# Kernel optimization log

Measured on AMD Instinct MI355X. Metric: run time of the kernel, lower is better.

## Reference

```python
import jax, jax.numpy as jnp
import numpy as np

N, F_IN, HID, HEADS, E, NG = 50000, 128, 64, 4, 800000, 64
NEG_SLOPE = 0.2


def gat_conv(x, src, dst, W, a_src, a_dst, bias, heads, out_ch, concat):
    n = x.shape[0]
    h = (x @ W).reshape(n, heads, out_ch)                     # [N,H,C]
    # per-node attention logits
    al_src = jnp.sum(h * a_src, axis=-1)                      # [N,H]
    al_dst = jnp.sum(h * a_dst, axis=-1)                      # [N,H]
    e = jax.nn.leaky_relu(al_src[src] + al_dst[dst], NEG_SLOPE)  # [E,H]
    # segment softmax over incoming edges of each destination node
    m = jax.ops.segment_max(e, dst, num_segments=n)           # [N,H]
    m = jnp.where(jnp.isfinite(m), m, 0.0)
    ex = jnp.exp(e - m[dst])
    denom = jax.ops.segment_sum(ex, dst, num_segments=n)      # [N,H]
    alpha = ex / (denom[dst] + 1e-16)                         # [E,H]
    # weighted scatter-sum of gathered source features
    out = jax.ops.segment_sum(h[src] * alpha[:, :, None], dst, num_segments=n)  # [N,H,C]
    if concat:
        out = out.reshape(n, heads * out_ch)
    else:
        out = out.mean(axis=1)
    return out + bias


def setup_inputs() -> dict:
    key = jax.random.key(0)
    ks = jax.random.split(key, 16)
    x = jax.random.normal(ks[0], (N, F_IN), dtype=jnp.float32)
    edge_index = jax.random.randint(ks[1], (2, E), 0, N, dtype=jnp.int32)
    batch = jnp.sort(jax.random.randint(ks[2], (N,), 0, NG, dtype=jnp.int32))
    s1 = 1.0 / np.sqrt(F_IN)
    s2 = 1.0 / np.sqrt(HID * HEADS)
    W1 = jax.random.uniform(ks[3], (F_IN, HEADS * HID), jnp.float32, -s1, s1)
    a_src1 = jax.random.uniform(ks[4], (HEADS, HID), jnp.float32, -s1, s1)
    a_dst1 = jax.random.uniform(ks[5], (HEADS, HID), jnp.float32, -s1, s1)
    b1 = jnp.zeros((HEADS * HID,), jnp.float32)
    W2 = jax.random.uniform(ks[6], (HEADS * HID, HID), jnp.float32, -s2, s2)
    a_src2 = jax.random.uniform(ks[7], (1, HID), jnp.float32, -s2, s2)
    a_dst2 = jax.random.uniform(ks[8], (1, HID), jnp.float32, -s2, s2)
    b2 = jnp.zeros((HID,), jnp.float32)
    s3 = 1.0 / np.sqrt(HID)
    fcW = jax.random.uniform(ks[9], (HID, 1), jnp.float32, -s3, s3)
    fcb = jax.random.uniform(ks[10], (1,), jnp.float32, -s3, s3)
    return {"x": x, "edge_index": edge_index, "batch": batch,
            "W1": W1, "a_src1": a_src1, "a_dst1": a_dst1, "b1": b1,
            "W2": W2, "a_src2": a_src2, "a_dst2": a_dst2, "b2": b2,
            "fcW": fcW, "fcb": fcb}


def reference(x, edge_index, batch, W1, a_src1, a_dst1, b1, W2, a_src2, a_dst2, b2, fcW, fcb):
    n = x.shape[0]
    # PyG GATConv default: add self-loops
    loop = jnp.arange(n, dtype=edge_index.dtype)
    src = jnp.concatenate([edge_index[0], loop])
    dst = jnp.concatenate([edge_index[1], loop])
    # dropout layers are identity at inference
    h = gat_conv(x, src, dst, W1, a_src1, a_dst1, b1, HEADS, HID, True)
    h = jax.nn.elu(h)
    h = gat_conv(h, src, dst, W2, a_src2, a_dst2, b2, 1, HID, False)
    h = jax.nn.elu(h)
    # global mean pool over graphs
    sums = jax.ops.segment_sum(h, batch, num_segments=NG)      # [NG,HID]
    cnts = jax.ops.segment_sum(jnp.ones((n,), h.dtype), batch, num_segments=NG)
    pooled = sums / jnp.maximum(cnts, 1.0)[:, None]
    out = pooled @ fcW + fcb                                    # [NG,1]
    return out.squeeze(-1)
```

## Files before the change

kernel.cpp:

```cpp
#include <hip/hip_runtime.h>
#include <hip/hip_fp16.h>
#include <cstddef>
#include <cstdint>


#define LOG2E 1.4426950408889634f
__device__ __forceinline__ float lrelu02(float x) { return x >= 0.f ? x : 0.2f * x; }
__device__ __forceinline__ float elu1(float x)    { return x > 0.f ? x : expm1f(x); }
__device__ __forceinline__ float fexp(float x)    { return exp2f(x * LOG2E); }

typedef _Float16 f16x8 __attribute__((ext_vector_type(8)));
typedef float    f32x4 __attribute__((ext_vector_type(4)));

__global__ void k_hist(const int* __restrict__ dst, int* __restrict__ cnt,
                       int* __restrict__ rank, int e) {
    int i = blockIdx.x * 256 + threadIdx.x;
    if (i < e) rank[i] = atomicAdd(&cnt[dst[i]], 1);
}

__global__ __launch_bounds__(1024) void k_scan1(const int* __restrict__ cnt,
                                                int* __restrict__ cscan,
                                                int* __restrict__ bsum, int n) {
    __shared__ int ws[16];
    const int t = threadIdx.x, lane = t & 63, wv = t >> 6;
    const int i = blockIdx.x * 1024 + t;
    int v = (i < n) ? cnt[i] : 0;
    int s = v;
#pragma unroll
    for (int d = 1; d < 64; d <<= 1) { int o = __shfl_up(s, d); if (lane >= d) s += o; }
    if (lane == 63) ws[wv] = s;
    __syncthreads();
    if (t < 16) {
        int xx = ws[t];
#pragma unroll
        for (int d = 1; d < 16; d <<= 1) { int o = __shfl_up(xx, d); if (t >= d) xx += o; }
        ws[t] = xx;
        if (t == 15) bsum[blockIdx.x] = xx;
    }
    __syncthreads();
    int incl = s + (wv > 0 ? ws[wv - 1] : 0);
    if (i < n) cscan[i] = incl;
}

__global__ __launch_bounds__(1024) void k_scan2(int* __restrict__ bsum, int nb) {
    __shared__ int ws[16];
    const int t = threadIdx.x, lane = t & 63, wv = t >> 6;
    int v = (t < nb) ? bsum[t] : 0;
    int s = v;
#pragma unroll
    for (int d = 1; d < 64; d <<= 1) { int o = __shfl_up(s, d); if (lane >= d) s += o; }
    if (lane == 63) ws[wv] = s;
    __syncthreads();
    if (t < 16) {
        int xx = ws[t];
#pragma unroll
        for (int d = 1; d < 16; d <<= 1) { int o = __shfl_up(xx, d); if (t >= d) xx += o; }
        ws[t] = xx;
    }
    __syncthreads();
    int incl = s + (wv > 0 ? ws[wv - 1] : 0);
    if (t < nb) bsum[t] = incl - v;
}

__global__ __launch_bounds__(1024) void k_scan3(const int* __restrict__ cscan,
                                                const int* __restrict__ bsum,
                                                int* __restrict__ rowptr, int n) {
    const int i = blockIdx.x * 1024 + threadIdx.x;
    if (i < n) rowptr[i + 1] = cscan[i] + bsum[blockIdx.x];
    if (i == 0) rowptr[0] = 0;
}

__global__ void k_scatter(const int* __restrict__ src, const int* __restrict__ dstArr,
                          const int* __restrict__ rank, const int* __restrict__ rowptr,
                          int* __restrict__ csr, int e) {
    int i = blockIdx.x * 256 + threadIdx.x;
    if (i < e) csr[rowptr[dstArr[i]] + rank[i]] = src[i];
}

__device__ __forceinline__ void packOne(const float* __restrict__ W, __half* __restrict__ Bp,
                                        int K, int N, int i) {
    int c = i & 15, q = (i >> 4) & 3, tnt = i >> 6;
    int nt = tnt % (N / 16), t = tnt / (N / 16);
    int k0 = t * 32 + q * 8, col = nt * 16 + c;
    __half tmp[8];
#pragma unroll
    for (int j = 0; j < 8; ++j) tmp[j] = __float2half(W[(size_t)(k0 + j) * N + col]);
    *reinterpret_cast<int4*>(Bp + (size_t)i * 8) = *reinterpret_cast<int4*>(tmp);
}

__global__ void k_packW(const float* __restrict__ W1, __half* __restrict__ B1,
                        const float* __restrict__ W2, __half* __restrict__ B2) {
    int i = blockIdx.x * 256 + threadIdx.x;
    if (i < 4096) packOne(W1, B1, 128, 256, i);
    else if (i < 4096 + 2048) packOne(W2, B2, 256, 64, i - 4096);
}

template <int K, int N, bool AF32, int HEADS_>
__global__ __launch_bounds__(256) void k_gemm_mfma(const void* __restrict__ Av,
                                                   const __half* __restrict__ Bp,
                                                   __half* __restrict__ C,
                                                   const float* __restrict__ a_src,
                                                   const float* __restrict__ a_dst,
                                                   float* __restrict__ als,
                                                   float* __restrict__ ald, int M) {
    constexpr int NT = N / 16, KT = K / 32;
    const int lane = threadIdx.x & 63;
    const int wv = threadIdx.x >> 6;
    const int row0 = (blockIdx.x * 4 + wv) * 16;
    if (row0 >= M) return;

    f32x4 acc[NT];
#pragma unroll
    for (int nt = 0; nt < NT; ++nt) acc[nt] = (f32x4){0.f, 0.f, 0.f, 0.f};

    const __half* Ah = (const __half*)Av;
    const float*  Af = (const float*)Av;
    const size_t arow = (size_t)(row0 + (lane & 15)) * K + (lane >> 4) * 8;
    const __half* Bb = Bp + (size_t)lane * 8;
#pragma unroll
    for (int t = 0; t < KT; ++t) {
        f16x8 a;
        if constexpr (AF32) {
            float4 u0 = *reinterpret_cast<const float4*>(Af + arow + t * 32);
            float4 u1 = *reinterpret_cast<const float4*>(Af + arow + t * 32 + 4);
            a[0] = (_Float16)u0.x; a[1] = (_Float16)u0.y;
            a[2] = (_Float16)u0.z; a[3] = (_Float16)u0.w;
            a[4] = (_Float16)u1.x; a[5] = (_Float16)u1.y;
            a[6] = (_Float16)u1.z; a[7] = (_Float16)u1.w;
        } else {
            a = *reinterpret_cast<const f16x8*>(Ah + arow + t * 32);
        }
#pragma unroll
        for (int nt = 0; nt < NT; ++nt) {
            f16x8 b = *reinterpret_cast<const f16x8*>(Bb + (size_t)(t * NT + nt) * 512);
            acc[nt] = __builtin_amdgcn_mfma_f32_16x16x32_f16(a, b, acc[nt], 0, 0, 0);
        }
    }
    const int r0 = row0 + (lane >> 4) * 4;
    const int cl = lane & 15;
#pragma unroll
    for (int nt = 0; nt < NT; ++nt) {
        int col = nt * 16 + cl;
#pragma unroll
        for (int j = 0; j < 4; ++j)
            C[(size_t)(r0 + j) * N + col] = __float2half(acc[nt][j]);
    }
    float av[NT], dv[NT];
#pragma unroll
    for (int nt = 0; nt < NT; ++nt) {
        av[nt] = a_src[nt * 16 + cl];
        dv[nt] = a_dst[nt * 16 + cl];
    }
    constexpr int NTH = NT / HEADS_;
#pragma unroll
    for (int j = 0; j < 4; ++j) {
#pragma unroll
        for (int h = 0; h < HEADS_; ++h) {
            float ps = 0.f, pd = 0.f;
#pragma unroll
            for (int t = 0; t < NTH; ++t) {
                ps = fmaf(acc[h * NTH + t][j], av[h * NTH + t], ps);
                pd = fmaf(acc[h * NTH + t][j], dv[h * NTH + t], pd);
            }
#pragma unroll
            for (int d = 1; d < 16; d <<= 1) { ps += __shfl_xor(ps, d); pd += __shfl_xor(pd, d); }
            if (cl == 0) {
                int r = r0 + j;
                als[(size_t)r * HEADS_ + h] = ps;
                ald[(size_t)r * HEADS_ + h] = pd;
            }
        }
    }
}

__device__ __forceinline__ void h4acc(float2 raw, float w, float& ax, float& ay,
                                      float& az, float& aw2) {
    __half2* q = reinterpret_cast<__half2*>(&raw);
    float2 lo = __half22float2(q[0]), hi = __half22float2(q[1]);
    ax = fmaf(w, lo.x, ax); ay = fmaf(w, lo.y, ay);
    az = fmaf(w, hi.x, az); aw2 = fmaf(w, hi.y, aw2);
}

__global__ void k_edge1(const __half* __restrict__ h1, const float* __restrict__ als,
                        const float* __restrict__ ald, const int* __restrict__ rowptr,
                        const int* __restrict__ csr, const float* __restrict__ b1,
                        __half* __restrict__ x2, int n) {
    const int lane = threadIdx.x & 63;
    const int node = (blockIdx.x << 2) + (threadIdx.x >> 6);
    if (node >= n) return;
    const int ch = lane * 4;
    const int e8 = lane & 7, h8 = (lane >> 3) & 3;
    const float adh8 = ald[node * 4 + h8];
    const int head = lane >> 4;
    const int wb = head << 3;
    float axA = 0.f, ayA = 0.f, azA = 0.f, awA = 0.f;
    float axB = 0.f, ayB = 0.f, azB = 0.f, awB = 0.f;
    float wsum = 0.f;
    const int beg = rowptr[node];
    const int deg = rowptr[node + 1] - beg;
    for (int base = 0; base <= deg; base += 8) {
        int s0 = (base + 0 < deg) ? csr[beg + base + 0] : node;
        int s1 = (base + 1 < deg) ? csr[beg + base + 1] : node;
        int s2 = (base + 2 < deg) ? csr[beg + base + 2] : node;
        int s3 = (base + 3 < deg) ? csr[beg + base + 3] : node;
        int s4 = (base + 4 < deg) ? csr[beg + base + 4] : node;
        int s5 = (base + 5 < deg) ? csr[beg + base + 5] : node;
        int s6 = (base + 6 < deg) ? csr[beg + base + 6] : node;
        int s7 = (base + 7 < deg) ? csr[beg + base + 7] : node;
        float2 r0 = *reinterpret_cast<const float2*>(h1 + (size_t)s0 * 256 + ch);
        float2 r1 = *reinterpret_cast<const float2*>(h1 + (size_t)s1 * 256 + ch);
        float2 r2 = *reinterpret_cast<const float2*>(h1 + (size_t)s2 * 256 + ch);
        float2 r3 = *reinterpret_cast<const float2*>(h1 + (size_t)s3 * 256 + ch);
        float2 r4 = *reinterpret_cast<const float2*>(h1 + (size_t)s4 * 256 + ch);
        float2 r5 = *reinterpret_cast<const float2*>(h1 + (size_t)s5 * 256 + ch);
        float2 r6 = *reinterpret_cast<const float2*>(h1 + (size_t)s6 * 256 + ch);
        float2 r7 = *reinterpret_cast<const float2*>(h1 + (size_t)s7 * 256 + ch);
        int se = s0;
        se = (e8 == 1) ? s1 : se; se = (e8 == 2) ? s2 : se; se = (e8 == 3) ? s3 : se;
        se = (e8 == 4) ? s4 : se; se = (e8 == 5) ? s5 : se; se = (e8 == 6) ? s6 : se;
        se = (e8 == 7) ? s7 : se;
        float myw = (base + e8 <= deg)
                        ? fexp(lrelu02(als[(size_t)se * 4 + h8] + adh8)) : 0.f;
        float w0 = __shfl(myw, wb + 0), w1 = __shfl(myw, wb + 1);
        float w2 = __shfl(myw, wb + 2), w3 = __shfl(myw, wb + 3);
        float w4 = __shfl(myw, wb + 4), w5 = __shfl(myw, wb + 5);
        float w6 = __shfl(myw, wb + 6), w7 = __shfl(myw, wb + 7);
        h4acc(r0, w0, axA, ayA, azA, awA);
        h4acc(r1, w1, axB, ayB, azB, awB);
        h4acc(r2, w2, axA, ayA, azA, awA);
        h4acc(r3, w3, axB, ayB, azB, awB);
        h4acc(r4, w4, axA, ayA, azA, awA);
        h4acc(r5, w5, axB, ayB, azB, awB);
        h4acc(r6, w6, axA, ayA, azA, awA);
        h4acc(r7, w7, axB, ayB, azB, awB);
        wsum += ((w0 + w1) + (w2 + w3)) + ((w4 + w5) + (w6 + w7));
    }
    float ax = axA + axB, ay = ayA + ayB, az = azA + azB, aw = awA + awB;
    const float inv = 1.f / (wsum + 1e-16f);
    float4 bv = *reinterpret_cast<const float4*>(b1 + ch);
    __half2 o0 = __floats2half2_rn(elu1(ax * inv + bv.x), elu1(ay * inv + bv.y));
    __half2 o1 = __floats2half2_rn(elu1(az * inv + bv.z), elu1(aw * inv + bv.w));
    int2 p;
    p.x = *reinterpret_cast<int*>(&o0);
    p.y = *reinterpret_cast<int*>(&o1);
    *reinterpret_cast<int2*>(x2 + (size_t)node * 256 + ch) = p;
}

__global__ void k_edge2(const __half* __restrict__ h2, const float* __restrict__ als,
                        const float* __restrict__ ald, const int* __restrict__ rowptr,
                        const int* __restrict__ csr, const float* __restrict__ b2,
                        float* __restrict__ out2, int n) {
    const int lane = threadIdx.x & 63;
    const int node = (blockIdx.x << 2) + (threadIdx.x >> 6);
    if (node >= n) return;
    const int e8 = lane & 7;
    const float adl = ald[node];
    float accA = 0.f, accB = 0.f, wsum = 0.f;
    const int beg = rowptr[node];
    const int deg = rowptr[node + 1] - beg;
    for (int base = 0; base <= deg; base += 8) {
        int s0 = (base + 0 < deg) ? csr[beg + base + 0] : node;
        int s1 = (base + 1 < deg) ? csr[beg + base + 1] : node;
        int s2 = (base + 2 < deg) ? csr[beg + base + 2] : node;
        int s3 = (base + 3 < deg) ? csr[beg + base + 3] : node;
        int s4 = (base + 4 < deg) ? csr[beg + base + 4] : node;
        int s5 = (base + 5 < deg) ? csr[beg + base + 5] : node;
        int s6 = (base + 6 < deg) ? csr[beg + base + 6] : node;
        int s7 = (base + 7 < deg) ? csr[beg + base + 7] : node;
        float v0 = __half2float(h2[(size_t)s0 * 64 + lane]);
        float v1 = __half2float(h2[(size_t)s1 * 64 + lane]);
        float v2 = __half2float(h2[(size_t)s2 * 64 + lane]);
        float v3 = __half2float(h2[(size_t)s3 * 64 + lane]);
        float v4 = __half2float(h2[(size_t)s4 * 64 + lane]);
        float v5 = __half2float(h2[(size_t)s5 * 64 + lane]);
        float v6 = __half2float(h2[(size_t)s6 * 64 + lane]);
        float v7 = __half2float(h2[(size_t)s7 * 64 + lane]);
        int se = s0;
        se = (e8 == 1) ? s1 : se; se = (e8 == 2) ? s2 : se; se = (e8 == 3) ? s3 : se;
        se = (e8 == 4) ? s4 : se; se = (e8 == 5) ? s5 : se; se = (e8 == 6) ? s6 : se;
        se = (e8 == 7) ? s7 : se;
        float myw = (base + e8 <= deg) ? fexp(lrelu02(als[se] + adl)) : 0.f;
        float w0 = __shfl(myw, 0), w1 = __shfl(myw, 1), w2 = __shfl(myw, 2), w3 = __shfl(myw, 3);
        float w4 = __shfl(myw, 4), w5 = __shfl(myw, 5), w6 = __shfl(myw, 6), w7 = __shfl(myw, 7);
        accA = fmaf(w0, v0, accA); accB = fmaf(w1, v1, accB);
        accA = fmaf(w2, v2, accA); accB = fmaf(w3, v3, accB);
        accA = fmaf(w4, v4, accA); accB = fmaf(w5, v5, accB);
        accA = fmaf(w6, v6, accA); accB = fmaf(w7, v7, accB);
        wsum += (w0 + w1 + w2 + w3) + (w4 + w5 + w6 + w7);
    }
    float acc = accA + accB;
    float o = acc / (wsum + 1e-16f) + b2[lane];
    out2[(size_t)node * 64 + lane] = elu1(o);
}

__global__ __launch_bounds__(1024) void k_pool(const float* __restrict__ out2,
                                               const int* __restrict__ batch,
                                               const float* __restrict__ fcW,
                                               const float* __restrict__ fcb,
                                               float* __restrict__ out, int n) {
    __shared__ float sbuf[16][64];
    const int g = blockIdx.x;
    const int lane = threadIdx.x & 63, wv = threadIdx.x >> 6;
    int lo0 = 0, hi0 = n;
    while (lo0 < hi0) { int mid = (lo0 + hi0) >> 1; if (batch[mid] < g) lo0 = mid + 1; else hi0 = mid; }
    int lo1 = lo0, hi1 = n;
    while (lo1 < hi1) { int mid = (lo1 + hi1) >> 1; if (batch[mid] < g + 1) lo1 = mid + 1; else hi1 = mid; }
    float s0 = 0.f, s1 = 0.f;
    int r = lo0 + wv;
    for (; r + 16 < lo1; r += 32) {
        s0 += out2[(size_t)r * 64 + lane];
        s1 += out2[(size_t)(r + 16) * 64 + lane];
    }
    if (r < lo1) s0 += out2[(size_t)r * 64 + lane];
    sbuf[wv][lane] = s0 + s1;
    __syncthreads();
    if (wv == 0) {
        float s = 0.f;
#pragma unroll
        for (int k = 0; k < 16; ++k) s += sbuf[k][lane];
        float cntf = (float)(lo1 - lo0);
        float pooled = s / fmaxf(cntf, 1.f);
        float v = pooled * fcW[lane];
#pragma unroll
        for (int d = 32; d; d >>= 1) v += __shfl_xor(v, d);
        if (lane == 0) out[g] = v + fcb[0];
    }
}

extern "C" void kernel_launch(void* const* d_in, const int* in_sizes, int n_in,
                              void* d_out, int out_size, void* d_ws, size_t ws_size,
                              hipStream_t stream) {
    const float* x      = (const float*)d_in[0];
    const int*   ei     = (const int*)  d_in[1];
    const int*   batch  = (const int*)  d_in[2];
    const float* W1     = (const float*)d_in[3];
    const float* a_src1 = (const float*)d_in[4];
    const float* a_dst1 = (const float*)d_in[5];
    const float* b1     = (const float*)d_in[6];
    const float* W2     = (const float*)d_in[7];
    const float* a_src2 = (const float*)d_in[8];
    const float* a_dst2 = (const float*)d_in[9];
    const float* b2     = (const float*)d_in[10];
    const float* fcW    = (const float*)d_in[11];
    const float* fcb    = (const float*)d_in[12];
    float* out = (float*)d_out;

    const int N = in_sizes[2];
    const int E = in_sizes[1] / 2;
    (void)n_in; (void)ws_size;

    char* ws = (char*)d_ws;
    size_t off = 0;
    auto alloc = [&](size_t bytes) -> char* {
        char* p = ws + off;
        off += (bytes + 255) & ~(size_t)255;
        return p;
    };
    int*    cnt    = (int*)   alloc((size_t)N * 4);
    int*    cscan  = (int*)   alloc((size_t)N * 4);
    int*    bsum   = (int*)   alloc((size_t)1024 * 4);
    int*    rank   = (int*)   alloc((size_t)E * 4);
    int*    rowptr = (int*)   alloc((size_t)(N + 1) * 4);
    int*    csr    = (int*)   alloc((size_t)(E + 8) * 4);
    __half* W1p    = (__half*)alloc((size_t)128 * 256 * 2);
    __half* W2p    = (__half*)alloc((size_t)256 * 64 * 2);
    __half* h1h    = (__half*)alloc((size_t)N * 256 * 2);
    __half* x2h    = (__half*)alloc((size_t)N * 256 * 2);
    __half* h2h    = (__half*)alloc((size_t)N * 64 * 2);
    float*  out2   = (float*) alloc((size_t)N * 64 * 4);
    float*  als1   = (float*) alloc((size_t)N * 4 * 4);
    float*  ald1   = (float*) alloc((size_t)N * 4 * 4);
    float*  als2   = (float*) alloc((size_t)N * 4);
    float*  ald2   = (float*) alloc((size_t)N * 4);

    hipMemsetAsync(cnt, 0, (size_t)N * 4, stream);
    const int ge = (E + 255) / 256;
    const int nb = (N + 1023) / 1024;
    k_hist<<<ge, 256, 0, stream>>>(ei + E, cnt, rank, E);
    k_scan1<<<nb, 1024, 0, stream>>>(cnt, cscan, bsum, N);
    k_scan2<<<1, 1024, 0, stream>>>(bsum, nb);
    k_scan3<<<nb, 1024, 0, stream>>>(cscan, bsum, rowptr, N);
    k_scatter<<<ge, 256, 0, stream>>>(ei, ei + E, rank, rowptr, csr, E);

    k_packW<<<24, 256, 0, stream>>>(W1, W1p, W2, W2p);

    const int gw = (N / 16 + 3) / 4;
    const int gn4 = (N + 3) / 4;
    k_gemm_mfma<128, 256, true, 4><<<gw, 256, 0, stream>>>(x, W1p, h1h,
                                                           a_src1, a_dst1, als1, ald1, N);
    k_edge1<<<gn4, 256, 0, stream>>>(h1h, als1, ald1, rowptr, csr, b1, x2h, N);

    k_gemm_mfma<256, 64, false, 1><<<gw, 256, 0, stream>>>(x2h, W2p, h2h,
                                                           a_src2, a_dst2, als2, ald2, N);
    k_edge2<<<gn4, 256, 0, stream>>>(h2h, als2, ald2, rowptr, csr, b2, out2, N);

    k_pool<<<out_size, 1024, 0, stream>>>(out2, batch, fcW, fcb, out, N);
}
```

Measured before the change: 218.2 us.

## Widen gather loads to 16 bytes and split edges across lane groups

```diff
diff --git a/kernel.cpp b/kernel.cpp
--- a/kernel.cpp
+++ b/kernel.cpp
@@ -173,12 +173,13 @@
     }
 }
 
-__device__ __forceinline__ void h4acc(float2 raw, float w, float& ax, float& ay,
-                                      float& az, float& aw2) {
-    __half2* q = reinterpret_cast<__half2*>(&raw);
-    float2 lo = __half22float2(q[0]), hi = __half22float2(q[1]);
-    ax = fmaf(w, lo.x, ax); ay = fmaf(w, lo.y, ay);
-    az = fmaf(w, hi.x, az); aw2 = fmaf(w, hi.y, aw2);
+__device__ __forceinline__ void h8acc(float4 v, float w, float* acc) {
+    const __half2* hv = reinterpret_cast<const __half2*>(&v);
+#pragma unroll
+    for (int c = 0; c < 4; ++c) {
+        acc[2 * c + 0] = fmaf(w, (float)__low2half(hv[c]),  acc[2 * c + 0]);
+        acc[2 * c + 1] = fmaf(w, (float)__high2half(hv[c]), acc[2 * c + 1]);
+    }
 }
 
 __global__ void k_edge1(const __half* __restrict__ h1, const float* __restrict__ als,
@@ -188,13 +189,12 @@
     const int lane = threadIdx.x & 63;
     const int node = (blockIdx.x << 2) + (threadIdx.x >> 6);
     if (node >= n) return;
-    const int ch = lane * 4;
+    const int eslot = lane >> 5;
+    const int ch8 = (lane & 31) * 8;
     const int e8 = lane & 7, h8 = (lane >> 3) & 3;
     const float adh8 = ald[node * 4 + h8];
-    const int head = lane >> 4;
-    const int wb = head << 3;
-    float axA = 0.f, ayA = 0.f, azA = 0.f, awA = 0.f;
-    float axB = 0.f, ayB = 0.f, azB = 0.f, awB = 0.f;
+    const int slbase = (((lane & 31) >> 3) << 3) + eslot;
+    float acc[8] = {0.f, 0.f, 0.f, 0.f, 0.f, 0.f, 0.f, 0.f};
     float wsum = 0.f;
     const int beg = rowptr[node];
     const int deg = rowptr[node + 1] - beg;
@@ -207,43 +207,51 @@
         int s5 = (base + 5 < deg) ? csr[beg + base + 5] : node;
         int s6 = (base + 6 < deg) ? csr[beg + base + 6] : node;
         int s7 = (base + 7 < deg) ? csr[beg + base + 7] : node;
-        float2 r0 = *reinterpret_cast<const float2*>(h1 + (size_t)s0 * 256 + ch);
-        float2 r1 = *reinterpret_cast<const float2*>(h1 + (size_t)s1 * 256 + ch);
-        float2 r2 = *reinterpret_cast<const float2*>(h1 + (size_t)s2 * 256 + ch);
-        float2 r3 = *reinterpret_cast<const float2*>(h1 + (size_t)s3 * 256 + ch);
-        float2 r4 = *reinterpret_cast<const float2*>(h1 + (size_t)s4 * 256 + ch);
-        float2 r5 = *reinterpret_cast<const float2*>(h1 + (size_t)s5 * 256 + ch);
-        float2 r6 = *reinterpret_cast<const float2*>(h1 + (size_t)s6 * 256 + ch);
-        float2 r7 = *reinterpret_cast<const float2*>(h1 + (size_t)s7 * 256 + ch);
+        int p0 = eslot ? s1 : s0;
+        int p1 = eslot ? s3 : s2;
+        int p2 = eslot ? s5 : s4;
+        int p3 = eslot ? s7 : s6;
+        float4 v0 = *reinterpret_cast<const float4*>(h1 + (size_t)p0 * 256 + ch8);
+        float4 v1 = *reinterpret_cast<const float4*>(h1 + (size_t)p1 * 256 + ch8);
+        float4 v2 = *reinterpret_cast<const float4*>(h1 + (size_t)p2 * 256 + ch8);
+        float4 v3 = *reinterpret_cast<const float4*>(h1 + (size_t)p3 * 256 + ch8);
         int se = s0;
         se = (e8 == 1) ? s1 : se; se = (e8 == 2) ? s2 : se; se = (e8 == 3) ? s3 : se;
         se = (e8 == 4) ? s4 : se; se = (e8 == 5) ? s5 : se; se = (e8 == 6) ? s6 : se;
         se = (e8 == 7) ? s7 : se;
         float myw = (base + e8 <= deg)
                         ? fexp(lrelu02(als[(size_t)se * 4 + h8] + adh8)) : 0.f;
-        float w0 = __shfl(myw, wb + 0), w1 = __shfl(myw, wb + 1);
-        float w2 = __shfl(myw, wb + 2), w3 = __shfl(myw, wb + 3);
-        float w4 = __shfl(myw, wb + 4), w5 = __shfl(myw, wb + 5);
-        float w6 = __shfl(myw, wb + 6), w7 = __shfl(myw, wb + 7);
-        h4acc(r0, w0, axA, ayA, azA, awA);
-        h4acc(r1, w1, axB, ayB, azB, awB);
-        h4acc(r2, w2, axA, ayA, azA, awA);
-        h4acc(r3, w3, axB, ayB, azB, awB);
-        h4acc(r4, w4, axA, ayA, azA, awA);
-        h4acc(r5, w5, axB, ayB, azB, awB);
-        h4acc(r6, w6, axA, ayA, azA, awA);
-        h4acc(r7, w7, axB, ayB, azB, awB);
-        wsum += ((w0 + w1) + (w2 + w3)) + ((w4 + w5) + (w6 + w7));
-    }
-    float ax = axA + axB, ay = ayA + ayB, az = azA + azB, aw = awA + awB;
-    const float inv = 1.f / (wsum + 1e-16f);
-    float4 bv = *reinterpret_cast<const float4*>(b1 + ch);
-    __half2 o0 = __floats2half2_rn(elu1(ax * inv + bv.x), elu1(ay * inv + bv.y));
-    __half2 o1 = __floats2half2_rn(elu1(az * inv + bv.z), elu1(aw * inv + bv.w));
-    int2 p;
-    p.x = *reinterpret_cast<int*>(&o0);
-    p.y = *reinterpret_cast<int*>(&o1);
-    *reinterpret_cast<int2*>(x2 + (size_t)node * 256 + ch) = p;
+        float w0 = __shfl(myw, slbase + 0);
+        float w1 = __shfl(myw, slbase + 2);
+        float w2 = __shfl(myw, slbase + 4);
+        float w3 = __shfl(myw, slbase + 6);
+        h8acc(v0, w0, acc);
+        h8acc(v1, w1, acc);
+        h8acc(v2, w2, acc);
+        h8acc(v3, w3, acc);
+        wsum += (w0 + w1) + (w2 + w3);
+    }
+#pragma unroll
+    for (int c = 0; c < 8; ++c) acc[c] += __shfl_xor(acc[c], 32);
+    wsum += __shfl_xor(wsum, 32);
+    if (eslot == 0) {
+        const float inv = 1.f / (wsum + 1e-16f);
+        float4 b0 = *reinterpret_cast<const float4*>(b1 + ch8);
+        float4 b4 = *reinterpret_cast<const float4*>(b1 + ch8 + 4);
+        float o[8];
+        o[0] = elu1(acc[0] * inv + b0.x); o[1] = elu1(acc[1] * inv + b0.y);
+        o[2] = elu1(acc[2] * inv + b0.z); o[3] = elu1(acc[3] * inv + b0.w);
+        o[4] = elu1(acc[4] * inv + b4.x); o[5] = elu1(acc[5] * inv + b4.y);
+        o[6] = elu1(acc[6] * inv + b4.z); o[7] = elu1(acc[7] * inv + b4.w);
+        __half2 q0 = __floats2half2_rn(o[0], o[1]);
+        __half2 q1 = __floats2half2_rn(o[2], o[3]);
+        __half2 q2 = __floats2half2_rn(o[4], o[5]);
+        __half2 q3 = __floats2half2_rn(o[6], o[7]);
+        int4 p;
+        p.x = *reinterpret_cast<int*>(&q0); p.y = *reinterpret_cast<int*>(&q1);
+        p.z = *reinterpret_cast<int*>(&q2); p.w = *reinterpret_cast<int*>(&q3);
+        *reinterpret_cast<int4*>(x2 + (size_t)node * 256 + ch8) = p;
+    }
 }
 
 __global__ void k_edge2(const __half* __restrict__ h2, const float* __restrict__ als,
@@ -253,9 +261,12 @@
     const int lane = threadIdx.x & 63;
     const int node = (blockIdx.x << 2) + (threadIdx.x >> 6);
     if (node >= n) return;
+    const int eslot = lane >> 3;
+    const int ch8 = (lane & 7) * 8;
     const int e8 = lane & 7;
     const float adl = ald[node];
-    float accA = 0.f, accB = 0.f, wsum = 0.f;
+    float acc[8] = {0.f, 0.f, 0.f, 0.f, 0.f, 0.f, 0.f, 0.f};
+    float wsum = 0.f;
     const int beg = rowptr[node];
     const int deg = rowptr[node + 1] - beg;
     for (int base = 0; base <= deg; base += 8) {
@@ -267,30 +278,40 @@
         int s5 = (base + 5 < deg) ? csr[beg + base + 5] : node;
         int s6 = (base + 6 < deg) ? csr[beg + base + 6] : node;
         int s7 = (base + 7 < deg) ? csr[beg + base + 7] : node;
-        float v0 = __half2float(h2[(size_t)s0 * 64 + lane]);
-        float v1 = __half2float(h2[(size_t)s1 * 64 + lane]);
-        float v2 = __half2float(h2[(size_t)s2 * 64 + lane]);
-        float v3 = __half2float(h2[(size_t)s3 * 64 + lane]);
-        float v4 = __half2float(h2[(size_t)s4 * 64 + lane]);
-        float v5 = __half2float(h2[(size_t)s5 * 64 + lane]);
-        float v6 = __half2float(h2[(size_t)s6 * 64 + lane]);
-        float v7 = __half2float(h2[(size_t)s7 * 64 + lane]);
+        int sp = s0;
+        sp = (eslot == 1) ? s1 : sp; sp = (eslot == 2) ? s2 : sp; sp = (eslot == 3) ? s3 : sp;
+        sp = (eslot == 4) ? s4 : sp; sp = (eslot == 5) ? s5 : sp; sp = (eslot == 6) ? s6 : sp;
+        sp = (eslot == 7) ? s7 : sp;
+        float4 v = *reinterpret_cast<const float4*>(h2 + (size_t)sp * 64 + ch8);
         int se = s0;
         se = (e8 == 1) ? s1 : se; se = (e8 == 2) ? s2 : se; se = (e8 == 3) ? s3 : se;
         se = (e8 == 4) ? s4 : se; se = (e8 == 5) ? s5 : se; se = (e8 == 6) ? s6 : se;
         se = (e8 == 7) ? s7 : se;
         float myw = (base + e8 <= deg) ? fexp(lrelu02(als[se] + adl)) : 0.f;
-        float w0 = __shfl(myw, 0), w1 = __shfl(myw, 1), w2 = __shfl(myw, 2), w3 = __shfl(myw, 3);
-        float w4 = __shfl(myw, 4), w5 = __shfl(myw, 5), w6 = __shfl(myw, 6), w7 = __shfl(myw, 7);
-        accA = fmaf(w0, v0, accA); accB = fmaf(w1, v1, accB);
-        accA = fmaf(w2, v2, accA); accB = fmaf(w3, v3, accB);
-        accA = fmaf(w4, v4, accA); accB = fmaf(w5, v5, accB);
-        accA = fmaf(w6, v6, accA); accB = fmaf(w7, v7, accB);
-        wsum += (w0 + w1 + w2 + w3) + (w4 + w5 + w6 + w7);
-    }
-    float acc = accA + accB;
-    float o = acc / (wsum + 1e-16f) + b2[lane];
-    out2[(size_t)node * 64 + lane] = elu1(o);
+        float w = __shfl(myw, eslot);
+        h8acc(v, w, acc);
+        wsum += w;
+    }
+#pragma unroll
+    for (int st = 8; st < 64; st <<= 1) {
+#pragma unroll
+        for (int c = 0; c < 8; ++c) acc[c] += __shfl_xor(acc[c], st);
+        wsum += __shfl_xor(wsum, st);
+    }
+    if (eslot == 0) {
+        const float inv = 1.f / (wsum + 1e-16f);
+        float4 o0, o1;
+        o0.x = elu1(acc[0] * inv + b2[ch8 + 0]);
+        o0.y = elu1(acc[1] * inv + b2[ch8 + 1]);
+        o0.z = elu1(acc[2] * inv + b2[ch8 + 2]);
+        o0.w = elu1(acc[3] * inv + b2[ch8 + 3]);
+        o1.x = elu1(acc[4] * inv + b2[ch8 + 4]);
+        o1.y = elu1(acc[5] * inv + b2[ch8 + 5]);
+        o1.z = elu1(acc[6] * inv + b2[ch8 + 6]);
+        o1.w = elu1(acc[7] * inv + b2[ch8 + 7]);
+        *reinterpret_cast<float4*>(out2 + (size_t)node * 64 + ch8) = o0;
+        *reinterpret_cast<float4*>(out2 + (size_t)node * 64 + ch8 + 4) = o1;
+    }
 }
 
 __global__ __launch_bounds__(1024) void k_pool(const float* __restrict__ out2,
```

Result: slower. 230.5 us (+5.6%).

## Split layer-1 aggregation into weight precompute and channel-sliced gather kernels

Applied to the files above, without the earlier changes.

```diff
diff --git a/kernel.cpp b/kernel.cpp
--- a/kernel.cpp
+++ b/kernel.cpp
@@ -173,31 +173,56 @@
     }
 }
 
-__device__ __forceinline__ void h4acc(float2 raw, float w, float& ax, float& ay,
-                                      float& az, float& aw2) {
-    __half2* q = reinterpret_cast<__half2*>(&raw);
-    float2 lo = __half22float2(q[0]), hi = __half22float2(q[1]);
-    ax = fmaf(w, lo.x, ax); ay = fmaf(w, lo.y, ay);
-    az = fmaf(w, hi.x, az); aw2 = fmaf(w, hi.y, aw2);
-}
-
-__global__ void k_edge1(const __half* __restrict__ h1, const float* __restrict__ als,
-                        const float* __restrict__ ald, const int* __restrict__ rowptr,
-                        const int* __restrict__ csr, const float* __restrict__ b1,
-                        __half* __restrict__ x2, int n) {
+__global__ void k_w1(const float* __restrict__ als, const float* __restrict__ ald,
+                     const int* __restrict__ rowptr, const int* __restrict__ csr,
+                     __half* __restrict__ wbuf, __half* __restrict__ selfw,
+                     float* __restrict__ inv1, int n, int epad) {
     const int lane = threadIdx.x & 63;
     const int node = (blockIdx.x << 2) + (threadIdx.x >> 6);
     if (node >= n) return;
-    const int ch = lane * 4;
+    const bool lo = lane < 32;
     const int e8 = lane & 7, h8 = (lane >> 3) & 3;
-    const float adh8 = ald[node * 4 + h8];
-    const int head = lane >> 4;
-    const int wb = head << 3;
-    float axA = 0.f, ayA = 0.f, azA = 0.f, awA = 0.f;
-    float axB = 0.f, ayB = 0.f, azB = 0.f, awB = 0.f;
-    float wsum = 0.f;
+    const float adh = ald[node * 4 + h8];
     const int beg = rowptr[node];
     const int deg = rowptr[node + 1] - beg;
+    float wsum = 0.f;
+    for (int base = 0; base < deg; base += 8) {
+        float w = 0.f;
+        if (lo && base + e8 < deg) {
+            int se = csr[beg + base + e8];
+            w = fexp(lrelu02(als[(size_t)se * 4 + h8] + adh));
+            wbuf[(size_t)h8 * epad + beg + base + e8] = __float2half(w);
+        }
+        wsum += w;
+    }
+    float ws = fexp(lrelu02(als[node * 4 + h8] + adh));
+    if (lo && e8 == 0) {
+        selfw[node * 4 + h8] = __float2half(ws);
+        wsum += ws;
+    }
+#pragma unroll
+    for (int d = 1; d < 8; d <<= 1) wsum += __shfl_xor(wsum, d);
+    if (lo && e8 == 0) inv1[node * 4 + h8] = 1.f / (wsum + 1e-16f);
+}
+
+__global__ void k_edge1s(const __half* __restrict__ h1, const __half* __restrict__ wbuf,
+                         const __half* __restrict__ selfw, const float* __restrict__ inv1,
+                         const int* __restrict__ rowptr, const int* __restrict__ csr,
+                         const float* __restrict__ b1, __half* __restrict__ x2,
+                         int n, int epad) {
+    const int lane = threadIdx.x & 63;
+    const int slice = blockIdx.x & 7;
+    const int node = (blockIdx.x >> 3) * 4 + (threadIdx.x >> 6);
+    if (node >= n) return;
+    const int head = slice >> 1;
+    const int chl = lane & 31;
+    const int eslot = lane >> 5;
+    const int e8 = lane & 7;
+    const __half* hb = h1 + slice * 32 + chl;
+    const int beg = rowptr[node];
+    const int deg = rowptr[node + 1] - beg;
+    const float wself = __half2float(selfw[node * 4 + head]);
+    float acc = 0.f;
     for (int base = 0; base <= deg; base += 8) {
         int s0 = (base + 0 < deg) ? csr[beg + base + 0] : node;
         int s1 = (base + 1 < deg) ? csr[beg + base + 1] : node;
@@ -207,43 +232,32 @@
         int s5 = (base + 5 < deg) ? csr[beg + base + 5] : node;
         int s6 = (base + 6 < deg) ? csr[beg + base + 6] : node;
         int s7 = (base + 7 < deg) ? csr[beg + base + 7] : node;
-        float2 r0 = *reinterpret_cast<const float2*>(h1 + (size_t)s0 * 256 + ch);
-        float2 r1 = *reinterpret_cast<const float2*>(h1 + (size_t)s1 * 256 + ch);
-        float2 r2 = *reinterpret_cast<const float2*>(h1 + (size_t)s2 * 256 + ch);
-        float2 r3 = *reinterpret_cast<const float2*>(h1 + (size_t)s3 * 256 + ch);
-        float2 r4 = *reinterpret_cast<const float2*>(h1 + (size_t)s4 * 256 + ch);
-        float2 r5 = *reinterpret_cast<const float2*>(h1 + (size_t)s5 * 256 + ch);
-        float2 r6 = *reinterpret_cast<const float2*>(h1 + (size_t)s6 * 256 + ch);
-        float2 r7 = *reinterpret_cast<const float2*>(h1 + (size_t)s7 * 256 + ch);
-        int se = s0;
-        se = (e8 == 1) ? s1 : se; se = (e8 == 2) ? s2 : se; se = (e8 == 3) ? s3 : se;
-        se = (e8 == 4) ? s4 : se; se = (e8 == 5) ? s5 : se; se = (e8 == 6) ? s6 : se;
-        se = (e8 == 7) ? s7 : se;
-        float myw = (base + e8 <= deg)
-                        ? fexp(lrelu02(als[(size_t)se * 4 + h8] + adh8)) : 0.f;
-        float w0 = __shfl(myw, wb + 0), w1 = __shfl(myw, wb + 1);
-        float w2 = __shfl(myw, wb + 2), w3 = __shfl(myw, wb + 3);
-        float w4 = __shfl(myw, wb + 4), w5 = __shfl(myw, wb + 5);
-        float w6 = __shfl(myw, wb + 6), w7 = __shfl(myw, wb + 7);
-        h4acc(r0, w0, axA, ayA, azA, awA);
-        h4acc(r1, w1, axB, ayB, azB, awB);
-        h4acc(r2, w2, axA, ayA, azA, awA);
-        h4acc(r3, w3, axB, ayB, azB, awB);
-        h4acc(r4, w4, axA, ayA, azA, awA);
-        h4acc(r5, w5, axB, ayB, azB, awB);
-        h4acc(r6, w6, axA, ayA, azA, awA);
-        h4acc(r7, w7, axB, ayB, azB, awB);
-        wsum += ((w0 + w1) + (w2 + w3)) + ((w4 + w5) + (w6 + w7));
-    }
-    float ax = axA + axB, ay = ayA + ayB, az = azA + azB, aw = awA + awB;
-    const float inv = 1.f / (wsum + 1e-16f);
-    float4 bv = *reinterpret_cast<const float4*>(b1 + ch);
-    __half2 o0 = __floats2half2_rn(elu1(ax * inv + bv.x), elu1(ay * inv + bv.y));
-    __half2 o1 = __floats2half2_rn(elu1(az * inv + bv.z), elu1(aw * inv + bv.w));
-    int2 p;
-    p.x = *reinterpret_cast<int*>(&o0);
-    p.y = *reinterpret_cast<int*>(&o1);
-    *reinterpret_cast<int2*>(x2 + (size_t)node * 256 + ch) = p;
+        float myw;
+        if (base + e8 < deg)       myw = __half2float(wbuf[(size_t)head * epad + beg + base + e8]);
+        else if (base + e8 == deg) myw = wself;
+        else                       myw = 0.f;
+        int p0 = eslot ? s1 : s0;
+        int p1 = eslot ? s3 : s2;
+        int p2 = eslot ? s5 : s4;
+        int p3 = eslot ? s7 : s6;
+        float v0 = __half2float(hb[(size_t)p0 * 256]);
+        float v1 = __half2float(hb[(size_t)p1 * 256]);
+        float v2 = __half2float(hb[(size_t)p2 * 256]);
+        float v3 = __half2float(hb[(size_t)p3 * 256]);
+        float w0 = __shfl(myw, 0 + eslot);
+        float w1 = __shfl(myw, 2 + eslot);
+        float w2 = __shfl(myw, 4 + eslot);
+        float w3 = __shfl(myw, 6 + eslot);
+        acc = fmaf(w0, v0, acc);
+        acc = fmaf(w1, v1, acc);
+        acc = fmaf(w2, v2, acc);
+        acc = fmaf(w3, v3, acc);
+    }
+    acc += __shfl_xor(acc, 32);
+    if (eslot == 0) {
+        float o = elu1(acc * inv1[node * 4 + head] + b1[slice * 32 + chl]);
+        x2[(size_t)node * 256 + slice * 32 + chl] = __float2half(o);
+    }
 }
 
 __global__ void k_edge2(const __half* __restrict__ h2, const float* __restrict__ als,
@@ -347,6 +361,7 @@
 
     const int N = in_sizes[2];
     const int E = in_sizes[1] / 2;
+    const int EPAD = E + 8;
     (void)n_in; (void)ws_size;
 
     char* ws = (char*)d_ws;
@@ -372,6 +387,9 @@
     float*  ald1   = (float*) alloc((size_t)N * 4 * 4);
     float*  als2   = (float*) alloc((size_t)N * 4);
     float*  ald2   = (float*) alloc((size_t)N * 4);
+    __half* wbuf   = (__half*)alloc((size_t)4 * EPAD * 2);
+    __half* selfw  = (__half*)alloc((size_t)N * 4 * 2);
+    float*  inv1   = (float*) alloc((size_t)N * 4 * 4);
 
     hipMemsetAsync(cnt, 0, (size_t)N * 4, stream);
     const int ge = (E + 255) / 256;
@@ -388,7 +406,9 @@
     const int gn4 = (N + 3) / 4;
     k_gemm_mfma<128, 256, true, 4><<<gw, 256, 0, stream>>>(x, W1p, h1h,
                                                            a_src1, a_dst1, als1, ald1, N);
-    k_edge1<<<gn4, 256, 0, stream>>>(h1h, als1, ald1, rowptr, csr, b1, x2h, N);
+    k_w1<<<gn4, 256, 0, stream>>>(als1, ald1, rowptr, csr, wbuf, selfw, inv1, N, EPAD);
+    k_edge1s<<<gn4 * 8, 256, 0, stream>>>(h1h, wbuf, selfw, inv1, rowptr, csr, b1, x2h,
+                                          N, EPAD);
 
     k_gemm_mfma<256, 64, false, 1><<<gw, 256, 0, stream>>>(x2h, W2p, h2h,
                                                            a_src2, a_dst2, als2, ald2, N);
```

After: 377.9 us. 1.73x slower.
